# Kernel optimization log

Measured on AMD Instinct MI355X. Metric: run time of the kernel, lower is better.

The kernel has to match this reference:

```python
import jax, jax.numpy as jnp
import numpy as np
import math

INF = 1e12  # constant.INFINITY_NUMBER in the original repo
B, T, D = 64, 512, 1024  # D = 2 * rnn_hidden


def _lin(k, fan_in, fan_out):
    k1, k2 = jax.random.split(k)
    w = jax.random.normal(k1, (fan_in, fan_out), jnp.float32) / np.float32(np.sqrt(fan_in))
    b = jax.random.normal(k2, (fan_out,), jnp.float32) * 0.01
    return w, b


def setup_inputs() -> dict:
    key = jax.random.key(0)
    ks = jax.random.split(key, 12)
    gcn_inputs = jax.random.normal(ks[0], (B, T, D), jnp.float32)
    subj_pos = jax.random.randint(ks[1], (B, T), 0, 8)  # zeros mark the subject span
    obj_pos = jax.random.randint(ks[2], (B, T), 0, 8)
    masks = jax.random.randint(ks[3], (B, T), 0, 2)
    Wq, bq = _lin(ks[4], 2 * D, D)
    Wc, bc = _lin(ks[5], 2 * D, D)
    Wk, bk = _lin(ks[6], D, 1)
    Wm, bm = _lin(ks[7], 3 * D, D)
    WK, bK = _lin(ks[8], D, D)
    WQ, bQ = _lin(ks[9], D, D)
    WV, bV = _lin(ks[10], D, D)
    return dict(gcn_inputs=gcn_inputs, subj_pos=subj_pos, obj_pos=obj_pos, masks=masks,
                Wq=Wq, bq=bq, Wc=Wc, bc=bc, Wk=Wk, bk=bk, Wm=Wm, bm=bm,
                WK=WK, bK=bK, WQ=WQ, bQ=bQ, WV=WV, bV=bV)


def _pool_max(h, mask):
    # mask: True = masked out
    return jnp.max(jnp.where(mask, jnp.float32(-INF), h), axis=1)


def reference(gcn_inputs, subj_pos, obj_pos, masks,
              Wq, bq, Wc, bc, Wk, bk, Wm, bm, WK, bK, WQ, bQ, WV, bV):
    b, t, d = gcn_inputs.shape
    scale = np.float32(1.0 / math.sqrt(d))

    subj_mask = (subj_pos != 0)[:, :, None]  # .eq(0).eq(0)
    subj_out = _pool_max(gcn_inputs, subj_mask)            # [B, D]
    obj_out = _pool_max(gcn_inputs, subj_mask)             # faithful: original also uses subj_mask here
    subj_obj = jnp.concatenate([subj_out, obj_out], axis=1)  # [B, 2D]

    c0 = jnp.zeros((b, d), gcn_inputs.dtype)
    q = jax.nn.relu(subj_obj @ Wq + bq)                    # [B, D]
    tvec = jax.nn.relu(jnp.concatenate([q, c0], axis=1) @ Wc + bc)  # [B, D]
    k = jax.nn.softmax((tvec[:, None, :] * gcn_inputs) @ Wk + bk, axis=1)  # [B, T, 1]
    c = jnp.sum(k * gcn_inputs, axis=1)                    # [B, D]
    m = jax.nn.relu(jnp.concatenate([c, subj_obj], axis=1) @ Wm + bm)[:, None, :]  # [B, 1, D]

    key_h = gcn_inputs @ WK + bK
    query_h = gcn_inputs @ WQ + bQ
    value_h = gcn_inputs @ WV + bV
    scores = jnp.einsum('btd,bsd->bts', key_h, query_h)    # key.bmm(query^T): [B, T, T]

    # att branch: softmax first, THEN scale (faithful to the original quirk)
    att = jax.nn.softmax(scores, axis=2) * scale
    eye = jnp.eye(t, dtype=bool)[None]
    att = jnp.where(eye, jnp.float32(0.0), att).sum(axis=2)  # [B, T]

    # output branch: scale inside softmax
    probs = jax.nn.softmax(scores * scale, axis=2)
    output = m * jnp.einsum('bts,bsd->btd', probs, value_h)  # gated attention output [B, T, D]

    return output, masks[:, :, None], gcn_inputs, att
```

## Files before the change

### kernel.cpp

```cpp
#include <hip/hip_runtime.h>
#include <hip/hip_bf16.h>

#define B_ 64
#define T_ 512
#define D_ 1024
#define NCH 8
#define TCH 64
#define PSTRIDE 12
#define MVKC 128

#define OUT0_OFF 0u
#define OUT1_OFF 33554432u
#define OUT2_OFF 33587200u
#define OUT3_OFF 67141632u

typedef __attribute__((ext_vector_type(8))) short short8;
typedef __attribute__((ext_vector_type(4))) short short4v;
typedef __attribute__((ext_vector_type(4))) float f32x4;

__device__ __forceinline__ short bf16_of(float x) {
    __hip_bfloat16 h = __float2bfloat16(x);
    return *reinterpret_cast<short*>(&h);
}

__device__ __forceinline__ void gload16(const void* g, void* l) {
    __builtin_amdgcn_global_load_lds(
        (__attribute__((address_space(1))) void*)(g),
        (__attribute__((address_space(3))) void*)(l), 16, 0, 0);
}

__global__ __launch_bounds__(256) void pool_part(const float* __restrict__ gcn,
                                                 const int* __restrict__ subj_pos,
                                                 float* __restrict__ part) {
    __shared__ int keep[TCH];
    int d = threadIdx.x * 4;
    int ch = blockIdx.y, b = blockIdx.z;
    if (threadIdx.x < TCH) keep[threadIdx.x] = (subj_pos[b * T_ + ch * TCH + threadIdx.x] == 0);
    __syncthreads();
    const float* gb = gcn + ((size_t)b * T_ + ch * TCH) * D_ + d;
    f32x4 mx = {-1e12f, -1e12f, -1e12f, -1e12f};
    #pragma unroll 4
    for (int i = 0; i < TCH; i++) {
        f32x4 v = *(const f32x4*)(gb + (size_t)i * D_);
        if (keep[i]) {
            mx[0] = fmaxf(mx[0], v[0]);
            mx[1] = fmaxf(mx[1], v[1]);
            mx[2] = fmaxf(mx[2], v[2]);
            mx[3] = fmaxf(mx[3], v[3]);
        }
    }
    *(f32x4*)(part + ((size_t)b * PSTRIDE + ch) * D_ + d) = mx;
}

__global__ __launch_bounds__(256) void pool_red(const float* __restrict__ part,
                                                float* __restrict__ subj) {
    int d = threadIdx.x * 4;
    int b = blockIdx.y;
    f32x4 mx = {-1e12f, -1e12f, -1e12f, -1e12f};
    #pragma unroll
    for (int ch = 0; ch < NCH; ch++) {
        f32x4 v = *(const f32x4*)(part + ((size_t)b * PSTRIDE + ch) * D_ + d);
        mx[0] = fmaxf(mx[0], v[0]);
        mx[1] = fmaxf(mx[1], v[1]);
        mx[2] = fmaxf(mx[2], v[2]);
        mx[3] = fmaxf(mx[3], v[3]);
    }
    *(f32x4*)(subj + (size_t)b * D_ + d) = mx;
}

__global__ __launch_bounds__(256) void mvg_part(const float* __restrict__ x0,
                                                const float* __restrict__ x1,
                                                const float* __restrict__ W,
                                                float* __restrict__ pmv) {
    __shared__ float xs[MVKC][64];
    __shared__ float ws[MVKC][64];
    int n0 = blockIdx.x * 64;
    int k0 = blockIdx.y * MVKC;
    for (int i = threadIdx.x; i < MVKC * 64; i += 256) {
        int k = i >> 6, b = i & 63;
        int kg = k0 + k;
        xs[k][b] = (kg < D_) ? x0[(size_t)b * D_ + kg]
                             : x1[(size_t)b * D_ + ((kg - D_) & (D_ - 1))];
    }
    for (int i = threadIdx.x; i < MVKC * 16; i += 256) {
        int r = i >> 4, c4 = (i & 15) * 4;
        *(f32x4*)&ws[r][c4] = *(const f32x4*)(W + (size_t)(k0 + r) * D_ + n0 + c4);
    }
    __syncthreads();
    int n = threadIdx.x & 63;
    int bg = (threadIdx.x >> 6) * 16;
    f32x4 acc[4] = {};
    for (int k = 0; k < MVKC; k++) {
        float wv = ws[k][n];
        #pragma unroll
        for (int g = 0; g < 4; g++) {
            f32x4 xv = *(const f32x4*)&xs[k][bg + g * 4];
            acc[g] += xv * wv;
        }
    }
    #pragma unroll
    for (int g = 0; g < 4; g++)
        #pragma unroll
        for (int q = 0; q < 4; q++)
            pmv[((size_t)blockIdx.y * 64 + bg + g * 4 + q) * D_ + n0 + n] = acc[g][q];
}

__global__ __launch_bounds__(256) void mvg_red(const float* __restrict__ pmv,
                                               const float* __restrict__ bias,
                                               float* __restrict__ y, int nkch) {
    int j = threadIdx.x * 4;
    int b = blockIdx.y;
    f32x4 acc = *(const f32x4*)(bias + j);
    for (int kch = 0; kch < nkch; kch++)
        acc += *(const f32x4*)(pmv + ((size_t)kch * 64 + b) * D_ + j);
    #pragma unroll
    for (int q = 0; q < 4; q++) acc[q] = fmaxf(acc[q], 0.f);
    *(f32x4*)(y + (size_t)b * D_ + j) = acc;
}

__global__ __launch_bounds__(256) void vecs_kernel(const float* __restrict__ WKm,
                                                   const float* __restrict__ WQm,
                                                   const float* __restrict__ bKv,
                                                   const float* __restrict__ bQv,
                                                   float* __restrict__ u,
                                                   float* __restrict__ w,
                                                   float* __restrict__ alpha) {
    int tid = threadIdx.x, wave = tid >> 6, lane = tid & 63;
    int row = blockIdx.x * 4 + wave;
    float s1 = 0.f, s2 = 0.f;
    for (int c = lane; c < D_; c += 64) {
        s1 += WKm[(size_t)row * D_ + c] * bQv[c];
        s2 += WQm[(size_t)row * D_ + c] * bKv[c];
    }
    #pragma unroll
    for (int off = 32; off; off >>= 1) {
        s1 += __shfl_xor(s1, off);
        s2 += __shfl_xor(s2, off);
    }
    if (lane == 0) { u[row] = s1; w[row] = s2; }
    if (blockIdx.x == 0 && wave == 0) {
        float a = 0.f;
        for (int c = lane; c < D_; c += 64) a += bKv[c] * bQv[c];
        #pragma unroll
        for (int off = 32; off; off >>= 1) a += __shfl_xor(a, off);
        if (lane == 0) alpha[0] = a;
    }
}

__global__ __launch_bounds__(256) void att_dots(const float* __restrict__ gcn,
                                                const float* __restrict__ u,
                                                const float* __restrict__ w,
                                                const float* __restrict__ tv,
                                                const float* __restrict__ Wk,
                                                const float* __restrict__ alpha,
                                                const float* __restrict__ bk,
                                                float* __restrict__ Gu,
                                                float* __restrict__ Gw,
                                                float* __restrict__ lg) {
    __shared__ float su[D_], sw[D_], s2[D_];
    int tid = threadIdx.x, wave = tid >> 6, lane = tid & 63;
    size_t row0 = (size_t)blockIdx.x * 4;
    int b = (int)(row0 >> 9);
    for (int c = tid; c < D_; c += 256) {
        su[c] = u[c];
        sw[c] = w[c];
        s2[c] = tv[(size_t)b * D_ + c] * Wk[c];
    }
    __syncthreads();
    size_t row = row0 + wave;
    const float* g = gcn + row * D_;
    float d1 = 0.f, d2 = 0.f, d3 = 0.f;
    #pragma unroll
    for (int it = 0; it < 4; it++) {
        int c = lane * 4 + it * 256;
        f32x4 gv = *(const f32x4*)(g + c);
        f32x4 uu = *(const f32x4*)(su + c);
        f32x4 ww = *(const f32x4*)(sw + c);
        f32x4 kk = *(const f32x4*)(s2 + c);
        #pragma unroll
        for (int q = 0; q < 4; q++) {
            d1 += gv[q] * uu[q];
            d2 += gv[q] * ww[q];
            d3 += gv[q] * kk[q];
        }
    }
    #pragma unroll
    for (int off = 32; off; off >>= 1) {
        d1 += __shfl_xor(d1, off);
        d2 += __shfl_xor(d2, off);
        d3 += __shfl_xor(d3, off);
    }
    if (lane == 0) {
        Gu[row] = d1 + alpha[0];
        Gw[row] = d2;
        lg[row] = d3 + bk[0];
    }
}

__global__ __launch_bounds__(256) void ksoftmax_kernel(float* __restrict__ lg) {
    __shared__ float red[4];
    int b = blockIdx.x, tid = threadIdx.x;
    int wave = tid >> 6, lane = tid & 63;
    float* L = lg + (size_t)b * T_;
    float v0 = L[tid], v1 = L[tid + 256];
    float mx = fmaxf(v0, v1);
    #pragma unroll
    for (int off = 32; off; off >>= 1) mx = fmaxf(mx, __shfl_xor(mx, off));
    if (lane == 0) red[wave] = mx;
    __syncthreads();
    mx = fmaxf(fmaxf(red[0], red[1]), fmaxf(red[2], red[3]));
    __syncthreads();
    float e0 = expf(v0 - mx), e1 = expf(v1 - mx);
    float zs = e0 + e1;
    #pragma unroll
    for (int off = 32; off; off >>= 1) zs += __shfl_xor(zs, off);
    if (lane == 0) red[wave] = zs;
    __syncthreads();
    float invZ = 1.f / (red[0] + red[1] + red[2] + red[3]);
    L[tid] = e0 * invZ;
    L[tid + 256] = e1 * invZ;
}

__global__ __launch_bounds__(256) void csum_part(const float* __restrict__ gcn,
                                                 const float* __restrict__ k,
                                                 float* __restrict__ part) {
    __shared__ float kv[TCH];
    int d = threadIdx.x * 4;
    int ch = blockIdx.y, b = blockIdx.z;
    if (threadIdx.x < TCH) kv[threadIdx.x] = k[(size_t)b * T_ + ch * TCH + threadIdx.x];
    __syncthreads();
    const float* gb = gcn + ((size_t)b * T_ + ch * TCH) * D_ + d;
    f32x4 acc = {};
    #pragma unroll 4
    for (int i = 0; i < TCH; i++) acc += kv[i] * *(const f32x4*)(gb + (size_t)i * D_);
    *(f32x4*)(part + ((size_t)b * PSTRIDE + ch) * D_ + d) = acc;
}

__global__ __launch_bounds__(256) void csum_reduce(const float* __restrict__ part,
                                                   float* __restrict__ cbuf) {
    int d = threadIdx.x * 4;
    int b = blockIdx.y;
    f32x4 acc = {};
    #pragma unroll
    for (int ch = 0; ch < NCH; ch++)
        acc += *(const f32x4*)(part + ((size_t)b * PSTRIDE + ch) * D_ + d);
    *(f32x4*)(cbuf + (size_t)b * D_ + d) = acc;
}

__global__ __launch_bounds__(256) void cast_kernel(const float* __restrict__ in,
                                                   short* __restrict__ out, size_t n8) {
    size_t i = (size_t)blockIdx.x * 256 + threadIdx.x;
    size_t stride = (size_t)gridDim.x * 256;
    for (; i < n8; i += stride) {
        f32x4 v0 = ((const f32x4*)in)[2 * i];
        f32x4 v1 = ((const f32x4*)in)[2 * i + 1];
        short8 o;
        #pragma unroll
        for (int j = 0; j < 4; j++) {
            o[j] = bf16_of(v0[j]);
            o[4 + j] = bf16_of(v1[j]);
        }
        ((short8*)out)[i] = o;
    }
}

__global__ __launch_bounds__(256) void prep_kernel(const float* __restrict__ in,
                                                   short* __restrict__ gs,
                                                   short* __restrict__ gt,
                                                   float* __restrict__ o2) {
    __shared__ float tile[32][33];
    int z = blockIdx.z;
    in += (size_t)z * T_ * D_;
    gs += (size_t)z * T_ * D_;
    gt += (size_t)z * D_ * T_;
    o2 += (size_t)z * T_ * D_;
    int c0 = blockIdx.x * 32, r0 = blockIdx.y * 32;
    int tx = threadIdx.x & 7, ty = threadIdx.x >> 3;
    {
        size_t idx = (size_t)(r0 + ty) * D_ + c0 + tx * 4;
        f32x4 v = *(const f32x4*)(in + idx);
        *(f32x4*)(o2 + idx) = v;
        short4v s;
        #pragma unroll
        for (int q = 0; q < 4; q++) {
            s[q] = bf16_of(v[q]);
            tile[ty][tx * 4 + q] = v[q];
        }
        *(short4v*)(gs + idx) = s;
    }
    __syncthreads();
    int tx2 = threadIdx.x & 31, ty2 = threadIdx.x >> 5;
    #pragma unroll
    for (int i = 0; i < 4; i++) {
        int c = ty2 + i * 8;
        gt[(size_t)(c0 + c) * T_ + r0 + tx2] = bf16_of(tile[tx2][c]);
    }
}

__global__ __launch_bounds__(256) void transpose_kernel(const float* __restrict__ in, size_t sIn,
                                                        short* __restrict__ out, size_t sOut,
                                                        int R, int C) {
    __shared__ float tile[32][33];
    int z = blockIdx.z;
    in += (size_t)z * sIn;
    out += (size_t)z * sOut;
    int c0 = blockIdx.x * 32, r0 = blockIdx.y * 32;
    int tx = threadIdx.x & 31, ty = threadIdx.x >> 5;
    #pragma unroll
    for (int i = 0; i < 4; i++) {
        int r = ty + i * 8;
        tile[r][tx] = in[(size_t)(r0 + r) * C + c0 + tx];
    }
    __syncthreads();
    #pragma unroll
    for (int i = 0; i < 4; i++) {
        int c = ty + i * 8;
        out[(size_t)(c0 + c) * R + r0 + tx] = bf16_of(tile[tx][c]);
    }
}

template <int MODE>
__global__ __launch_bounds__(256) void gemm_nt(
        const short* __restrict__ A, size_t sAz,
        const short* __restrict__ Bt, size_t sBz,
        int K, int ldout,
        float* __restrict__ Cf, short* __restrict__ Cb, size_t sCz,
        const float* __restrict__ e1, const float* __restrict__ e2) {
    __shared__ __align__(16) short As[128 * 64];
    __shared__ __align__(16) short Bs[128 * 64];
    unsigned gx = gridDim.x, gy = gridDim.y;
    unsigned lin = blockIdx.x + gx * (blockIdx.y + gy * blockIdx.z);
    unsigned tot = gx * gy * gridDim.z;
    unsigned swz = (lin & 7u) * (tot >> 3) + (lin >> 3);
    unsigned bx = swz % gx;
    unsigned tmp = swz / gx;
    unsigned by = tmp % gy;
    unsigned bz = tmp / gy;

    int z = bz;
    A += (size_t)z * sAz;
    Bt += (size_t)z * sBz;
    int t = threadIdx.x;
    int lane = t & 63, wave = t >> 6;
    int wr = wave >> 1, wc = wave & 1;
    size_t rowBase = (size_t)bx * 128;
    size_t colBase = (size_t)by * 128;

    int rlo = lane >> 3;
    int src16 = (lane & 7) ^ rlo;
    const short* gA[4];
    const short* gB[4];
    short* lA[4];
    short* lB[4];
    #pragma unroll
    for (int i = 0; i < 4; i++) {
        int ch = wave * 4 + i;
        int row = ch * 8 + rlo;
        gA[i] = A + (rowBase + row) * (size_t)K + src16 * 8;
        gB[i] = Bt + (colBase + row) * (size_t)K + src16 * 8;
        lA[i] = As + ch * 512;
        lB[i] = Bs + ch * 512;
    }

    f32x4 acc[4][4] = {};
    for (int kb = 0; kb < K; kb += 64) {
        __syncthreads();
        #pragma unroll
        for (int i = 0; i < 4; i++) {
            gload16(gA[i] + kb, lA[i]);
            gload16(gB[i] + kb, lB[i]);
        }
        __syncthreads();
        #pragma unroll
        for (int kk = 0; kk < 2; kk++) {
            int ko16 = kk * 4 + (lane >> 4);
            int sw = ko16 ^ (lane & 7);
            short8 af[4], bfr[4];
            #pragma unroll
            for (int i = 0; i < 4; i++) {
                int row = wr * 64 + i * 16 + (lane & 15);
                af[i] = *(const short8*)(As + row * 64 + (sw << 3));
            }
            #pragma unroll
            for (int j = 0; j < 4; j++) {
                int row = wc * 64 + j * 16 + (lane & 15);
                bfr[j] = *(const short8*)(Bs + row * 64 + (sw << 3));
            }
            #pragma unroll
            for (int i = 0; i < 4; i++)
                #pragma unroll
                for (int j = 0; j < 4; j++)
                    acc[i][j] = __builtin_amdgcn_mfma_f32_16x16x32_bf16(af[i], bfr[j], acc[i][j], 0, 0, 0);
        }
    }
    #pragma unroll
    for (int i = 0; i < 4; i++) {
        #pragma unroll
        for (int j = 0; j < 4; j++) {
            #pragma unroll
            for (int r = 0; r < 4; r++) {
                size_t row = rowBase + wr * 64 + i * 16 + (lane >> 4) * 4 + r;
                size_t col = colBase + wc * 64 + j * 16 + (lane & 15);
                float v = acc[i][j][r];
                if (MODE == 0) {
                    Cf[z * sCz + row * ldout + col] = v;
                } else if (MODE == 1) {
                    Cf[z * sCz + row * ldout + col] = v + e1[z * T_ + row] + e2[z * T_ + col];
                } else if (MODE == 2) {
                    Cb[z * sCz + row * ldout + col] = bf16_of(v);
                } else {
                    Cf[z * sCz + row * ldout + col] = (v + e1[col]) * e2[(size_t)z * D_ + col];
                }
            }
        }
    }
}

__global__ __launch_bounds__(256) void softmax_att(const float* __restrict__ S,
                                                   short* __restrict__ probs,
                                                   float* __restrict__ att) {
    const float SCALE = 0.03125f;
    int wave = threadIdx.x >> 6, lane = threadIdx.x & 63;
    int t = blockIdx.x * 4 + wave, z = blockIdx.y;
    const float* row = S + ((size_t)z * T_ + t) * T_;
    short* prow = probs + ((size_t)z * T_ + t) * T_;
    float v[8];
    float mx = -1e30f;
    #pragma unroll
    for (int k = 0; k < 8; k++) {
        v[k] = row[lane + k * 64];
        mx = fmaxf(mx, v[k]);
    }
    #pragma unroll
    for (int off = 32; off; off >>= 1) mx = fmaxf(mx, __shfl_xor(mx, off));
    float z1 = 0.f, z2 = 0.f, dg = 0.f;
    #pragma unroll
    for (int k = 0; k < 8; k++) {
        float x = v[k] - mx;
        float e1 = expf(x);
        float e2 = expf(x * SCALE);
        z1 += e1;
        z2 += e2;
        if (lane + k * 64 == t) dg = e1;
        v[k] = e2;
    }
    #pragma unroll
    for (int off = 32; off; off >>= 1) {
        z1 += __shfl_xor(z1, off);
        z2 += __shfl_xor(z2, off);
        dg += __shfl_xor(dg, off);
    }
    float inv2 = 1.f / z2;
    #pragma unroll
    for (int k = 0; k < 8; k++) prow[lane + k * 64] = bf16_of(v[k] * inv2);
    if (lane == 0) att[z * T_ + t] = SCALE * (1.f - dg / z1);
}

__global__ __launch_bounds__(256) void masks_kernel(const int* __restrict__ masks,
                                                    float* __restrict__ out_masks) {
    int i = blockIdx.x * 256 + threadIdx.x;
    if (i < B_ * T_) out_masks[i] = (float)masks[i];
}

extern "C" void kernel_launch(void* const* d_in, const int* in_sizes, int n_in,
                              void* d_out, int out_size, void* d_ws, size_t ws_size,
                              hipStream_t stream) {
    const float* gcn = (const float*)d_in[0];
    const int* subj_pos = (const int*)d_in[1];
    const int* masks = (const int*)d_in[3];
    const float* Wq = (const float*)d_in[4];
    const float* bq = (const float*)d_in[5];
    const float* Wc = (const float*)d_in[6];
    const float* bc = (const float*)d_in[7];
    const float* Wk = (const float*)d_in[8];
    const float* bk = (const float*)d_in[9];
    const float* Wm = (const float*)d_in[10];
    const float* bm = (const float*)d_in[11];
    const float* WK = (const float*)d_in[12];
    const float* bK = (const float*)d_in[13];
    const float* WQ = (const float*)d_in[14];
    const float* bQ = (const float*)d_in[15];
    const float* WV = (const float*)d_in[16];
    const float* bV = (const float*)d_in[17];

    float* out = (float*)d_out;

    char* p = (char*)d_ws;
    auto alloc = [&](size_t bytes) {
        char* r = p;
        p += (bytes + 255) & ~(size_t)255;
        return r;
    };
    float* subj = (float*)alloc(B_ * D_ * 4);
    float* qv   = (float*)alloc(B_ * D_ * 4);
    float* tv   = (float*)alloc(B_ * D_ * 4);
    float* cb   = (float*)alloc(B_ * D_ * 4);
    float* mb   = (float*)alloc(B_ * D_ * 4);
    float* u    = (float*)alloc(D_ * 4);
    float* w    = (float*)alloc(D_ * 4);
    float* alph = (float*)alloc(256);
    float* Gu   = (float*)alloc(B_ * T_ * 4);
    float* Gw   = (float*)alloc(B_ * T_ * 4);
    float* lg   = (float*)alloc(B_ * T_ * 4);
    float* part = (float*)alloc((size_t)B_ * PSTRIDE * D_ * 4);
    float* pmv  = (float*)alloc((size_t)24 * 64 * D_ * 4);
    float* Pt   = (float*)alloc((size_t)D_ * D_ * 4);
    short* WKb  = (short*)alloc((size_t)D_ * D_ * 2);
    short* WQb  = (short*)alloc((size_t)D_ * D_ * 2);
    short* Ptb  = (short*)alloc((size_t)D_ * D_ * 2);
    short* WVt  = (short*)alloc((size_t)D_ * D_ * 2);

    size_t fixedBytes = (size_t)(p - (char*)d_ws);
    const size_t perBatch = (size_t)T_ * D_ * 2
                          + (size_t)T_ * D_ * 2
                          + (size_t)D_ * T_ * 2
                          + (size_t)T_ * T_ * 4
                          + (size_t)T_ * T_ * 2
                          + (size_t)T_ * D_ * 2;
    int nc = 64;
    while (nc > 1 && fixedBytes + (size_t)nc * perBatch + 4096 > ws_size) nc >>= 1;

    short* Gs_c    = (short*)alloc((size_t)nc * T_ * D_ * 2);
    short* Ys_c    = (short*)alloc((size_t)nc * T_ * D_ * 2);
    short* Gt_c    = (short*)alloc((size_t)nc * D_ * T_ * 2);
    float* S_c     = (float*)alloc((size_t)nc * T_ * T_ * 4);
    short* probs_c = (short*)alloc((size_t)nc * T_ * T_ * 2);
    short* Zs_c    = (short*)alloc((size_t)nc * T_ * D_ * 2);

    pool_part<<<dim3(1, NCH, B_), 256, 0, stream>>>(gcn, subj_pos, part);
    pool_red<<<dim3(1, B_), 256, 0, stream>>>(part, subj);
    mvg_part<<<dim3(D_ / 64, 16), 256, 0, stream>>>(subj, subj, Wq, pmv);
    mvg_red<<<dim3(1, B_), 256, 0, stream>>>(pmv, bq, qv, 16);
    mvg_part<<<dim3(D_ / 64, 8), 256, 0, stream>>>(qv, qv, Wc, pmv);
    mvg_red<<<dim3(1, B_), 256, 0, stream>>>(pmv, bc, tv, 8);
    vecs_kernel<<<D_ / 4, 256, 0, stream>>>(WK, WQ, bK, bQ, u, w, alph);
    att_dots<<<B_ * T_ / 4, 256, 0, stream>>>(gcn, u, w, tv, Wk, alph, bk, Gu, Gw, lg);
    ksoftmax_kernel<<<B_, 256, 0, stream>>>(lg);
    csum_part<<<dim3(1, NCH, B_), 256, 0, stream>>>(gcn, lg, part);
    csum_reduce<<<dim3(1, B_), 256, 0, stream>>>(part, cb);
    mvg_part<<<dim3(D_ / 64, 24), 256, 0, stream>>>(cb, subj, Wm, pmv);
    mvg_red<<<dim3(1, B_), 256, 0, stream>>>(pmv, bm, mb, 24);

    cast_kernel<<<512, 256, 0, stream>>>(WK, WKb, (size_t)D_ * D_ / 8);
    cast_kernel<<<512, 256, 0, stream>>>(WQ, WQb, (size_t)D_ * D_ / 8);
    gemm_nt<0><<<dim3(8, 8, 1), 256, 0, stream>>>(WQb, 0, WKb, 0, D_, D_,
                                                  Pt, nullptr, 0, nullptr, nullptr);
    cast_kernel<<<512, 256, 0, stream>>>(Pt, Ptb, (size_t)D_ * D_ / 8);
    transpose_kernel<<<dim3(32, 32, 1), 256, 0, stream>>>(WV, 0, WVt, 0, D_, D_);

    for (int b0 = 0; b0 < B_; b0 += nc) {
        const float* Gc = gcn + (size_t)b0 * T_ * D_;
        prep_kernel<<<dim3(D_ / 32, T_ / 32, nc), 256, 0, stream>>>(
            Gc, Gs_c, Gt_c, out + OUT2_OFF + (size_t)b0 * T_ * D_);
        gemm_nt<2><<<dim3(nc * T_ / 128, D_ / 128, 1), 256, 0, stream>>>(
            Gs_c, 0, Ptb, 0, D_, D_, nullptr, Ys_c, 0, nullptr, nullptr);
        gemm_nt<1><<<dim3(T_ / 128, T_ / 128, nc), 256, 0, stream>>>(
            Ys_c, (size_t)T_ * D_, Gs_c, (size_t)T_ * D_, D_, T_,
            S_c, nullptr, (size_t)T_ * T_, Gu + (size_t)b0 * T_, Gw + (size_t)b0 * T_);
        softmax_att<<<dim3(T_ / 4, nc), 256, 0, stream>>>(S_c, probs_c, out + OUT3_OFF + (size_t)b0 * T_);
        gemm_nt<2><<<dim3(T_ / 128, D_ / 128, nc), 256, 0, stream>>>(
            probs_c, (size_t)T_ * T_, Gt_c, (size_t)D_ * T_, T_, D_,
            nullptr, Zs_c, (size_t)T_ * D_, nullptr, nullptr);
        gemm_nt<3><<<dim3(T_ / 128, D_ / 128, nc), 256, 0, stream>>>(
            Zs_c, (size_t)T_ * D_, WVt, 0, D_, D_,
            out + OUT0_OFF + (size_t)b0 * T_ * D_, nullptr, (size_t)T_ * D_,
            bV, mb + (size_t)b0 * D_);
    }

    masks_kernel<<<(B_ * T_ + 255) / 256, 256, 0, stream>>>(masks, out + OUT1_OFF);
}
```

Baseline: 608.8 us.

## Fuse max-pooling into prep pass and read bf16 copies in reductions

```diff
diff --git a/kernel.cpp b/kernel.cpp
--- a/kernel.cpp
+++ b/kernel.cpp
@@ -6,7 +6,6 @@
 #define D_ 1024
 #define NCH 8
 #define TCH 64
-#define PSTRIDE 12
 #define MVKC 128
 
 #define OUT0_OFF 0u
@@ -22,6 +21,12 @@
     __hip_bfloat16 h = __float2bfloat16(x);
     return *reinterpret_cast<short*>(&h);
 }
+__device__ __forceinline__ float f32_of(short s) {
+    unsigned u = (unsigned)(unsigned short)s << 16;
+    float f;
+    __builtin_memcpy(&f, &u, 4);
+    return f;
+}
 
 __device__ __forceinline__ void gload16(const void* g, void* l) {
     __builtin_amdgcn_global_load_lds(
@@ -29,37 +34,59 @@
         (__attribute__((address_space(3))) void*)(l), 16, 0, 0);
 }
 
-__global__ __launch_bounds__(256) void pool_part(const float* __restrict__ gcn,
-                                                 const int* __restrict__ subj_pos,
-                                                 float* __restrict__ part) {
-    __shared__ int keep[TCH];
-    int d = threadIdx.x * 4;
-    int ch = blockIdx.y, b = blockIdx.z;
-    if (threadIdx.x < TCH) keep[threadIdx.x] = (subj_pos[b * T_ + ch * TCH + threadIdx.x] == 0);
-    __syncthreads();
-    const float* gb = gcn + ((size_t)b * T_ + ch * TCH) * D_ + d;
-    f32x4 mx = {-1e12f, -1e12f, -1e12f, -1e12f};
-    #pragma unroll 4
-    for (int i = 0; i < TCH; i++) {
-        f32x4 v = *(const f32x4*)(gb + (size_t)i * D_);
-        if (keep[i]) {
-            mx[0] = fmaxf(mx[0], v[0]);
-            mx[1] = fmaxf(mx[1], v[1]);
-            mx[2] = fmaxf(mx[2], v[2]);
-            mx[3] = fmaxf(mx[3], v[3]);
-        }
-    }
-    *(f32x4*)(part + ((size_t)b * PSTRIDE + ch) * D_ + d) = mx;
-}
-
-__global__ __launch_bounds__(256) void pool_red(const float* __restrict__ part,
+__global__ __launch_bounds__(256) void prep_kernel(const float* __restrict__ in,
+                                                   const int* __restrict__ subj_pos,
+                                                   short* __restrict__ gs,
+                                                   short* __restrict__ gt,
+                                                   float* __restrict__ o2,
+                                                   float* __restrict__ pmax) {
+    __shared__ float tile[32][33];
+    __shared__ int keep[32];
+    int z = blockIdx.z;
+    int c0 = blockIdx.x * 32, r0 = blockIdx.y * 32;
+    const float* inz = in + (size_t)z * T_ * D_;
+    short* gsz = gs + (size_t)z * T_ * D_;
+    short* gtz = gt + (size_t)z * D_ * T_;
+    float* o2z = o2 + (size_t)z * T_ * D_;
+    if (threadIdx.x < 32) keep[threadIdx.x] = (subj_pos[z * T_ + r0 + threadIdx.x] == 0);
+    int tx = threadIdx.x & 7, ty = threadIdx.x >> 3;
+    {
+        size_t idx = (size_t)(r0 + ty) * D_ + c0 + tx * 4;
+        f32x4 v = *(const f32x4*)(inz + idx);
+        *(f32x4*)(o2z + idx) = v;
+        short4v s;
+        #pragma unroll
+        for (int q = 0; q < 4; q++) {
+            s[q] = bf16_of(v[q]);
+            tile[ty][tx * 4 + q] = v[q];
+        }
+        *(short4v*)(gsz + idx) = s;
+    }
+    __syncthreads();
+    int tx2 = threadIdx.x & 31, ty2 = threadIdx.x >> 5;
+    #pragma unroll
+    for (int i = 0; i < 4; i++) {
+        int c = ty2 + i * 8;
+        gtz[(size_t)(c0 + c) * T_ + r0 + tx2] = bf16_of(tile[tx2][c]);
+    }
+    if (threadIdx.x < 32) {
+        int c = threadIdx.x;
+        float mx = -1e12f;
+        #pragma unroll 4
+        for (int r = 0; r < 32; r++)
+            if (keep[r]) mx = fmaxf(mx, tile[r][c]);
+        pmax[((size_t)z * 16 + (r0 >> 5)) * D_ + c0 + c] = mx;
+    }
+}
+
+__global__ __launch_bounds__(256) void pool_red(const float* __restrict__ pmax,
                                                 float* __restrict__ subj) {
     int d = threadIdx.x * 4;
     int b = blockIdx.y;
     f32x4 mx = {-1e12f, -1e12f, -1e12f, -1e12f};
     #pragma unroll
-    for (int ch = 0; ch < NCH; ch++) {
-        f32x4 v = *(const f32x4*)(part + ((size_t)b * PSTRIDE + ch) * D_ + d);
+    for (int ch = 0; ch < 16; ch++) {
+        f32x4 v = *(const f32x4*)(pmax + ((size_t)b * 16 + ch) * D_ + d);
         mx[0] = fmaxf(mx[0], v[0]);
         mx[1] = fmaxf(mx[1], v[1]);
         mx[2] = fmaxf(mx[2], v[2]);
@@ -147,7 +174,7 @@
     }
 }
 
-__global__ __launch_bounds__(256) void att_dots(const float* __restrict__ gcn,
+__global__ __launch_bounds__(256) void att_dots(const short* __restrict__ gs,
                                                 const float* __restrict__ u,
                                                 const float* __restrict__ w,
                                                 const float* __restrict__ tv,
@@ -168,20 +195,18 @@
     }
     __syncthreads();
     size_t row = row0 + wave;
-    const float* g = gcn + row * D_;
+    const short* g = gs + row * D_;
     float d1 = 0.f, d2 = 0.f, d3 = 0.f;
     #pragma unroll
     for (int it = 0; it < 4; it++) {
         int c = lane * 4 + it * 256;
-        f32x4 gv = *(const f32x4*)(g + c);
-        f32x4 uu = *(const f32x4*)(su + c);
-        f32x4 ww = *(const f32x4*)(sw + c);
-        f32x4 kk = *(const f32x4*)(s2 + c);
+        short4v gv = *(const short4v*)(g + c);
         #pragma unroll
         for (int q = 0; q < 4; q++) {
-            d1 += gv[q] * uu[q];
-            d2 += gv[q] * ww[q];
-            d3 += gv[q] * kk[q];
+            float gq = f32_of(gv[q]);
+            d1 += gq * su[c + q];
+            d2 += gq * sw[c + q];
+            d3 += gq * s2[c + q];
         }
     }
     #pragma unroll
@@ -221,7 +246,7 @@
     L[tid + 256] = e1 * invZ;
 }
 
-__global__ __launch_bounds__(256) void csum_part(const float* __restrict__ gcn,
+__global__ __launch_bounds__(256) void csum_part(const short* __restrict__ gs,
                                                  const float* __restrict__ k,
                                                  float* __restrict__ part) {
     __shared__ float kv[TCH];
@@ -229,11 +254,15 @@
     int ch = blockIdx.y, b = blockIdx.z;
     if (threadIdx.x < TCH) kv[threadIdx.x] = k[(size_t)b * T_ + ch * TCH + threadIdx.x];
     __syncthreads();
-    const float* gb = gcn + ((size_t)b * T_ + ch * TCH) * D_ + d;
+    const short* gb = gs + ((size_t)b * T_ + ch * TCH) * D_ + d;
     f32x4 acc = {};
     #pragma unroll 4
-    for (int i = 0; i < TCH; i++) acc += kv[i] * *(const f32x4*)(gb + (size_t)i * D_);
-    *(f32x4*)(part + ((size_t)b * PSTRIDE + ch) * D_ + d) = acc;
+    for (int i = 0; i < TCH; i++) {
+        short4v gv = *(const short4v*)(gb + (size_t)i * D_);
+        #pragma unroll
+        for (int q = 0; q < 4; q++) acc[q] += kv[i] * f32_of(gv[q]);
+    }
+    *(f32x4*)(part + ((size_t)b * NCH + ch) * D_ + d) = acc;
 }
 
 __global__ __launch_bounds__(256) void csum_reduce(const float* __restrict__ part,
@@ -243,7 +272,7 @@
     f32x4 acc = {};
     #pragma unroll
     for (int ch = 0; ch < NCH; ch++)
-        acc += *(const f32x4*)(part + ((size_t)b * PSTRIDE + ch) * D_ + d);
+        acc += *(const f32x4*)(part + ((size_t)b * NCH + ch) * D_ + d);
     *(f32x4*)(cbuf + (size_t)b * D_ + d) = acc;
 }
 
@@ -261,39 +290,6 @@
             o[4 + j] = bf16_of(v1[j]);
         }
         ((short8*)out)[i] = o;
-    }
-}
-
-__global__ __launch_bounds__(256) void prep_kernel(const float* __restrict__ in,
-                                                   short* __restrict__ gs,
-                                                   short* __restrict__ gt,
-                                                   float* __restrict__ o2) {
-    __shared__ float tile[32][33];
-    int z = blockIdx.z;
-    in += (size_t)z * T_ * D_;
-    gs += (size_t)z * T_ * D_;
-    gt += (size_t)z * D_ * T_;
-    o2 += (size_t)z * T_ * D_;
-    int c0 = blockIdx.x * 32, r0 = blockIdx.y * 32;
-    int tx = threadIdx.x & 7, ty = threadIdx.x >> 3;
-    {
-        size_t idx = (size_t)(r0 + ty) * D_ + c0 + tx * 4;
-        f32x4 v = *(const f32x4*)(in + idx);
-        *(f32x4*)(o2 + idx) = v;
-        short4v s;
-        #pragma unroll
-        for (int q = 0; q < 4; q++) {
-            s[q] = bf16_of(v[q]);
-            tile[ty][tx * 4 + q] = v[q];
-        }
-        *(short4v*)(gs + idx) = s;
-    }
-    __syncthreads();
-    int tx2 = threadIdx.x & 31, ty2 = threadIdx.x >> 5;
-    #pragma unroll
-    for (int i = 0; i < 4; i++) {
-        int c = ty2 + i * 8;
-        gt[(size_t)(c0 + c) * T_ + r0 + tx2] = bf16_of(tile[tx2][c]);
     }
 }
 
@@ -502,41 +498,42 @@
     float* Gu   = (float*)alloc(B_ * T_ * 4);
     float* Gw   = (float*)alloc(B_ * T_ * 4);
     float* lg   = (float*)alloc(B_ * T_ * 4);
-    float* part = (float*)alloc((size_t)B_ * PSTRIDE * D_ * 4);
+    float* part = (float*)alloc((size_t)B_ * NCH * D_ * 4);
+    float* pmax = (float*)alloc((size_t)B_ * 16 * D_ * 4);
     float* pmv  = (float*)alloc((size_t)24 * 64 * D_ * 4);
     float* Pt   = (float*)alloc((size_t)D_ * D_ * 4);
     short* WKb  = (short*)alloc((size_t)D_ * D_ * 2);
     short* WQb  = (short*)alloc((size_t)D_ * D_ * 2);
     short* Ptb  = (short*)alloc((size_t)D_ * D_ * 2);
     short* WVt  = (short*)alloc((size_t)D_ * D_ * 2);
+    short* Gs   = (short*)alloc((size_t)B_ * T_ * D_ * 2);
+    short* Gt   = (short*)alloc((size_t)B_ * D_ * T_ * 2);
 
     size_t fixedBytes = (size_t)(p - (char*)d_ws);
     const size_t perBatch = (size_t)T_ * D_ * 2
-                          + (size_t)T_ * D_ * 2
-                          + (size_t)D_ * T_ * 2
                           + (size_t)T_ * T_ * 4
                           + (size_t)T_ * T_ * 2
                           + (size_t)T_ * D_ * 2;
     int nc = 64;
     while (nc > 1 && fixedBytes + (size_t)nc * perBatch + 4096 > ws_size) nc >>= 1;
 
-    short* Gs_c    = (short*)alloc((size_t)nc * T_ * D_ * 2);
     short* Ys_c    = (short*)alloc((size_t)nc * T_ * D_ * 2);
-    short* Gt_c    = (short*)alloc((size_t)nc * D_ * T_ * 2);
     float* S_c     = (float*)alloc((size_t)nc * T_ * T_ * 4);
     short* probs_c = (short*)alloc((size_t)nc * T_ * T_ * 2);
     short* Zs_c    = (short*)alloc((size_t)nc * T_ * D_ * 2);
 
-    pool_part<<<dim3(1, NCH, B_), 256, 0, stream>>>(gcn, subj_pos, part);
-    pool_red<<<dim3(1, B_), 256, 0, stream>>>(part, subj);
+    prep_kernel<<<dim3(D_ / 32, T_ / 32, B_), 256, 0, stream>>>(
+        gcn, subj_pos, Gs, Gt, out + OUT2_OFF, pmax);
+
+    pool_red<<<dim3(1, B_), 256, 0, stream>>>(pmax, subj);
     mvg_part<<<dim3(D_ / 64, 16), 256, 0, stream>>>(subj, subj, Wq, pmv);
     mvg_red<<<dim3(1, B_), 256, 0, stream>>>(pmv, bq, qv, 16);
     mvg_part<<<dim3(D_ / 64, 8), 256, 0, stream>>>(qv, qv, Wc, pmv);
     mvg_red<<<dim3(1, B_), 256, 0, stream>>>(pmv, bc, tv, 8);
     vecs_kernel<<<D_ / 4, 256, 0, stream>>>(WK, WQ, bK, bQ, u, w, alph);
-    att_dots<<<B_ * T_ / 4, 256, 0, stream>>>(gcn, u, w, tv, Wk, alph, bk, Gu, Gw, lg);
+    att_dots<<<B_ * T_ / 4, 256, 0, stream>>>(Gs, u, w, tv, Wk, alph, bk, Gu, Gw, lg);
     ksoftmax_kernel<<<B_, 256, 0, stream>>>(lg);
-    csum_part<<<dim3(1, NCH, B_), 256, 0, stream>>>(gcn, lg, part);
+    csum_part<<<dim3(1, NCH, B_), 256, 0, stream>>>(Gs, lg, part);
     csum_reduce<<<dim3(1, B_), 256, 0, stream>>>(part, cb);
     mvg_part<<<dim3(D_ / 64, 24), 256, 0, stream>>>(cb, subj, Wm, pmv);
     mvg_red<<<dim3(1, B_), 256, 0, stream>>>(pmv, bm, mb, 24);
@@ -549,17 +546,16 @@
     transpose_kernel<<<dim3(32, 32, 1), 256, 0, stream>>>(WV, 0, WVt, 0, D_, D_);
 
     for (int b0 = 0; b0 < B_; b0 += nc) {
-        const float* Gc = gcn + (size_t)b0 * T_ * D_;
-        prep_kernel<<<dim3(D_ / 32, T_ / 32, nc), 256, 0, stream>>>(
-            Gc, Gs_c, Gt_c, out + OUT2_OFF + (size_t)b0 * T_ * D_);
+        const short* Gsc = Gs + (size_t)b0 * T_ * D_;
+        const short* Gtc = Gt + (size_t)b0 * D_ * T_;
         gemm_nt<2><<<dim3(nc * T_ / 128, D_ / 128, 1), 256, 0, stream>>>(
-            Gs_c, 0, Ptb, 0, D_, D_, nullptr, Ys_c, 0, nullptr, nullptr);
+            Gsc, 0, Ptb, 0, D_, D_, nullptr, Ys_c, 0, nullptr, nullptr);
         gemm_nt<1><<<dim3(T_ / 128, T_ / 128, nc), 256, 0, stream>>>(
-            Ys_c, (size_t)T_ * D_, Gs_c, (size_t)T_ * D_, D_, T_,
+            Ys_c, (size_t)T_ * D_, Gsc, (size_t)T_ * D_, D_, T_,
             S_c, nullptr, (size_t)T_ * T_, Gu + (size_t)b0 * T_, Gw + (size_t)b0 * T_);
         softmax_att<<<dim3(T_ / 4, nc), 256, 0, stream>>>(S_c, probs_c, out + OUT3_OFF + (size_t)b0 * T_);
         gemm_nt<2><<<dim3(T_ / 128, D_ / 128, nc), 256, 0, stream>>>(
-            probs_c, (size_t)T_ * T_, Gt_c, (size_t)D_ * T_, T_, D_,
+            probs_c, (size_t)T_ * T_, Gtc, (size_t)D_ * T_, T_, D_,
             nullptr, Zs_c, (size_t)T_ * D_, nullptr, nullptr);
         gemm_nt<3><<<dim3(T_ / 128, D_ / 128, nc), 256, 0, stream>>>(
             Zs_c, (size_t)T_ * D_, WVt, 0, D_, D_,
```

Result: faster. 567.9 us (-6.7%).
